# Kernel optimization log

Hardware: AMD Instinct MI355X
Metric: run time of the kernel (lower is better)

Reference implementation:

```python
import jax, jax.numpy as jnp
import numpy as np

FEATURE_DIM = 128

def setup_inputs() -> dict:
    key0 = jax.random.key(0)
    k1, k2, k3 = jax.random.split(key0, 3)
    B, NQ, NK, D = 4, 4096, 4096, FEATURE_DIM
    return {
        "target": jax.random.normal(k1, (B, NQ, D), dtype=jnp.float32),
        "key": jax.random.normal(k2, (B, NK, D), dtype=jnp.float32),
        "value": jax.random.normal(k3, (B, NK, D), dtype=jnp.float32),
    }

def reference(target, key, value):
    # Lan_K F: scores = target @ key^T / sqrt(d); weights = softmax(scores); out = weights @ value
    scale = 1.0 / np.sqrt(FEATURE_DIM).astype(np.float32)
    scores = jnp.einsum('bqd,bkd->bqk', target, key) * scale  # [B, NQ, NK]
    weights = jax.nn.softmax(scores, axis=-1)
    return jnp.einsum('bqk,bkd->bqd', weights, value)  # [B, NQ, D]
```

## Files before the change

kernel.cpp:

```cpp
#include <hip/hip_runtime.h>
#include <stdint.h>

#define B_ 4
#define NQ_ 4096
#define NK_ 4096
#define D_ 128
#define BM_ 64
#define BN_ 128
#define NITER_ (NK_/BN_)
#define KVBUF_ 32768
#define OS_ 66

typedef __attribute__((ext_vector_type(8))) short short8;
typedef __attribute__((ext_vector_type(4))) float floatx4;
typedef unsigned int u32;

union frag_u { u32 u[4]; short8 s; };

__device__ __forceinline__ unsigned short f2bf_rne(float x){
  union { float f; u32 u; } c; c.f = x;
  u32 u = c.u;
  return (unsigned short)((u + 0x7fffu + ((u >> 16) & 1u)) >> 16);
}
__device__ __forceinline__ u32 pk2bf(float a, float b){
  union { float f; u32 u; } x, y; x.f = a; y.f = b;
  u32 lo = (x.u + 0x7fffu + ((x.u >> 16) & 1u)) >> 16;
  u32 hi = (y.u + 0x7fffu + ((y.u >> 16) & 1u)) >> 16;
  return lo | (hi << 16);
}
__device__ __forceinline__ u32 pk2bf_t(float a, float b){
  union { float f; u32 u; } x, y; x.f = a; y.f = b;
  return (x.u >> 16) | (y.u & 0xffff0000u);
}

#define GLD16(gp, lp) __builtin_amdgcn_global_load_lds( \
    (const __attribute__((address_space(1))) u32*)(gp),  \
    (__attribute__((address_space(3))) u32*)(lp), 16, 0, 0)

__global__ void prep_kernel(const float* __restrict__ k, const float* __restrict__ v,
                            unsigned short* __restrict__ kb, unsigned short* __restrict__ vt){
  const int t = threadIdx.x;
  if (blockIdx.x >= 128){
    int base = (blockIdx.x - 128) * 2048 + t;
    #pragma unroll
    for (int i = 0; i < 8; i++){
      int j = base + i*256;
      float4 val = ((const float4*)k)[j];
      ushort4 s;
      s.x = f2bf_rne(val.x); s.y = f2bf_rne(val.y);
      s.z = f2bf_rne(val.z); s.w = f2bf_rne(val.w);
      ((ushort4*)kb)[j] = s;
    }
    return;
  }
  __shared__ __align__(16) float tile[128*128];
  const int b = blockIdx.x >> 5, kt = blockIdx.x & 31, k0 = kt*128;
  const float* vb = v + ((size_t)b*NK_ + k0)*D_;
  #pragma unroll
  for (int i = 0; i < 16; i++){
    int f = i*256 + t;
    int row = f >> 5, s4 = f & 31;
    *(float4*)(tile + row*128 + ((s4 ^ (row>>2)) << 2)) = *(const float4*)(vb + row*D_ + (s4<<2));
  }
  __syncthreads();
  unsigned short* vtb = vt + (size_t)b*D_*NK_ + k0;
  #pragma unroll
  for (int i = 0; i < 16; i++){
    int d = (t>>5) + 8*i, kq = t & 31;
    int s4 = d >> 2, e = d & 3;
    float v0 = tile[(4*kq+0)*128 + ((s4 ^ kq) << 2) + e];
    float v1 = tile[(4*kq+1)*128 + ((s4 ^ kq) << 2) + e];
    float v2 = tile[(4*kq+2)*128 + ((s4 ^ kq) << 2) + e];
    float v3 = tile[(4*kq+3)*128 + ((s4 ^ kq) << 2) + e];
    ushort4 o;
    o.x = f2bf_rne(v0); o.y = f2bf_rne(v1); o.z = f2bf_rne(v2); o.w = f2bf_rne(v3);
    *(ushort4*)(vtb + (size_t)d*NK_ + 4*kq) = o;
  }
}

__global__ __launch_bounds__(512, 2) void attn_kernel(
    const float* __restrict__ Qf, const unsigned short* __restrict__ Kb,
    const unsigned short* __restrict__ Vt, float* __restrict__ Out){
  __shared__ __align__(16) char sm[149504];
  char* smKb = sm;
  char* smVb = sm + 2*KVBUF_;
  char* smP  = sm + 4*KVBUF_;
  float* smL = (float*)(sm + 4*KVBUF_ + 16384);
  float* smO = (float*)sm;

  const int bi = blockIdx.x;
  const int b  = (bi >> 1) & 3;
  const int qt = ((bi >> 3) << 1) | (bi & 1);
  const int q0 = qt * BM_;
  const int tid = threadIdx.x;
  const int w = tid >> 6, lane = tid & 63;
  const int kg = w >> 1, dh = w & 1;
  const int l15 = lane & 15, l4 = lane >> 4;

  const unsigned short* kgb = Kb + (size_t)b * NK_ * D_;
  const unsigned short* vgb = Vt + (size_t)b * D_ * NK_;

  const int sr = lane >> 4;
  const int ssl = lane & 15;

  #pragma unroll
  for (int i = 0; i < 4; i++){
    int c = w*4 + i;
    int sg = ssl ^ (sr + 4*(c & 1));
    GLD16(kgb + (size_t)(c*4 + sr)*D_ + sg*8, smKb + c*1024);
    GLD16(vgb + (size_t)(c*4 + sr)*NK_ + sg*8, smVb + c*1024);
  }

  short8 qf[4][4];
  {
    const float* qp = Qf + ((size_t)b*NQ_ + q0)*D_;
    #pragma unroll
    for (int nb = 0; nb < 4; nb++)
      #pragma unroll
      for (int kb = 0; kb < 4; kb++){
        const float* p = qp + (size_t)(nb*16 + l15)*D_ + kb*32 + l4*8;
        float4 a = *(const float4*)p;
        float4 c4 = *(const float4*)(p + 4);
        frag_u f;
        f.u[0] = pk2bf(a.x, a.y);  f.u[1] = pk2bf(a.z, a.w);
        f.u[2] = pk2bf(c4.x, c4.y); f.u[3] = pk2bf(c4.z, c4.w);
        qf[nb][kb] = f.s;
      }
  }

  int koffs[4], voffs[4];
  {
    int row = kg*32 + dh*16 + l15;
    int c = row >> 2, r = row & 3, X = r + 4*(c & 1);
    #pragma unroll
    for (int k = 0; k < 4; k++)
      koffs[k] = c*1024 + r*256 + ((4*k + l4) ^ X)*16;
  }
  #pragma unroll
  for (int dt = 0; dt < 4; dt++){
    int d = dh*64 + dt*16 + l15;
    int c = d >> 2, r = d & 3, X = r + 4*(c & 1);
    voffs[dt] = c*1024 + r*256 + ((kg*4 + l4) ^ X)*16;
  }
  const int pwoff = l15*256 + (((kg*8 + dh*4 + l4) ^ (2*(l15 & 7))) * 8);
  const int proff = l15*256 + (((kg*4 + l4) ^ (l15 & 7)) * 16);

  floatx4 o[4][4];
  #pragma unroll
  for (int nb = 0; nb < 4; nb++)
    #pragma unroll
    for (int dt = 0; dt < 4; dt++) o[nb][dt] = (floatx4)0.0f;
  float lsum[4] = {0.f, 0.f, 0.f, 0.f};

  const float SL = 0.08838834764831845f * 1.4426950408889634f;

  __syncthreads();

  for (int it = 0; it < NITER_; ++it){
    const int buf = it & 1;
    char* kcur = smKb + buf * KVBUF_;
    char* vcur = smVb + buf * KVBUF_;

    if (it + 1 < NITER_){
      char* knxt = smKb + (buf ^ 1) * KVBUF_;
      #pragma unroll
      for (int i = 0; i < 4; i++){
        int c = w*4 + i;
        int sg = ssl ^ (sr + 4*(c & 1));
        GLD16(kgb + (size_t)((it+1)*BN_ + c*4 + sr)*D_ + sg*8, knxt + c*1024);
      }
    }

    short8 kf[4];
    kf[0] = *(const short8*)(kcur + koffs[0]);
    kf[1] = *(const short8*)(kcur + koffs[1]);
    kf[2] = *(const short8*)(kcur + koffs[2]);
    kf[3] = *(const short8*)(kcur + koffs[3]);
    floatx4 s[4];
    #pragma unroll
    for (int nb = 0; nb < 4; nb++){
      s[nb] = (floatx4)0.0f;
      s[nb] = __builtin_amdgcn_mfma_f32_16x16x32_bf16(kf[0], qf[nb][0], s[nb], 0,0,0);
      s[nb] = __builtin_amdgcn_mfma_f32_16x16x32_bf16(kf[1], qf[nb][1], s[nb], 0,0,0);
      s[nb] = __builtin_amdgcn_mfma_f32_16x16x32_bf16(kf[2], qf[nb][2], s[nb], 0,0,0);
      s[nb] = __builtin_amdgcn_mfma_f32_16x16x32_bf16(kf[3], qf[nb][3], s[nb], 0,0,0);
    }

    #pragma unroll
    for (int nb = 0; nb < 4; nb++){
      float p0 = __builtin_amdgcn_exp2f(s[nb][0] * SL);
      float p1 = __builtin_amdgcn_exp2f(s[nb][1] * SL);
      float p2 = __builtin_amdgcn_exp2f(s[nb][2] * SL);
      float p3 = __builtin_amdgcn_exp2f(s[nb][3] * SL);
      lsum[nb] += (p0 + p1) + (p2 + p3);
      uint2 pp; pp.x = pk2bf_t(p0, p1); pp.y = pk2bf_t(p2, p3);
      *(uint2*)(smP + nb*4096 + pwoff) = pp;
    }

    __syncthreads();

    if (it + 1 < NITER_){
      char* vnxt = smVb + (buf ^ 1) * KVBUF_;
      #pragma unroll
      for (int i = 0; i < 4; i++){
        int c = w*4 + i;
        int sg = ssl ^ (sr + 4*(c & 1));
        GLD16(vgb + (size_t)(c*4 + sr)*NK_ + (it+1)*BN_ + sg*8, vnxt + c*1024);
      }
    }

    short8 pf[4], vf[4];
    #pragma unroll
    for (int nb = 0; nb < 4; nb++)
      pf[nb] = *(const short8*)(smP + nb*4096 + proff);
    #pragma unroll
    for (int dt = 0; dt < 4; dt++)
      vf[dt] = *(const short8*)(vcur + voffs[dt]);
    #pragma unroll
    for (int nb = 0; nb < 4; nb++)
      #pragma unroll
      for (int dt = 0; dt < 4; dt++)
        o[nb][dt] = __builtin_amdgcn_mfma_f32_16x16x32_bf16(pf[nb], vf[dt], o[nb][dt], 0,0,0);

    __syncthreads();
  }

  #pragma unroll
  for (int nb = 0; nb < 4; nb++){
    float v = lsum[nb];
    v += __shfl_xor(v, 16);
    v += __shfl_xor(v, 32);
    lsum[nb] = v;
  }
  if (l4 == 0)
    #pragma unroll
    for (int nb = 0; nb < 4; nb++)
      smL[w*64 + nb*16 + l15] = lsum[nb];

  if (w >= 4){
    float* r = smO + (size_t)(w - 4) * 4224;
    #pragma unroll
    for (int nb = 0; nb < 4; nb++)
      #pragma unroll
      for (int dt = 0; dt < 4; dt++)
        #pragma unroll
        for (int q = 0; q < 4; q++)
          r[(size_t)(nb*16 + l4*4 + q)*OS_ + dt*16 + l15] = o[nb][dt][q];
  }
  __syncthreads();
  if (w < 4){
    float* r = smO + (size_t)w * 4224;
    #pragma unroll
    for (int nb = 0; nb < 4; nb++)
      #pragma unroll
      for (int dt = 0; dt < 4; dt++)
        #pragma unroll
        for (int q = 0; q < 4; q++)
          o[nb][dt][q] += r[(size_t)(nb*16 + l4*4 + q)*OS_ + dt*16 + l15];
  }
  __syncthreads();
  if (w == 2 || w == 3){
    float* r = smO + (size_t)(w - 2) * 4224;
    #pragma unroll
    for (int nb = 0; nb < 4; nb++)
      #pragma unroll
      for (int dt = 0; dt < 4; dt++)
        #pragma unroll
        for (int q = 0; q < 4; q++)
          r[(size_t)(nb*16 + l4*4 + q)*OS_ + dt*16 + l15] = o[nb][dt][q];
  }
  __syncthreads();
  if (w < 2){
    float* r = smO + (size_t)w * 4224;
    float* og = Out + ((size_t)b*NQ_ + q0)*D_ + dh*64;
    #pragma unroll
    for (int nb = 0; nb < 4; nb++)
      #pragma unroll
      for (int q = 0; q < 4; q++){
        int row = nb*16 + l4*4 + q;
        float lt = 0.f;
        #pragma unroll
        for (int w2 = 0; w2 < 8; w2++) lt += smL[w2*64 + row];
        float inv = 1.0f / lt;
        #pragma unroll
        for (int dt = 0; dt < 4; dt++){
          float val = o[nb][dt][q] + r[(size_t)row*OS_ + dt*16 + l15];
          og[(size_t)row*D_ + dt*16 + l15] = val * inv;
        }
      }
  }
}

extern "C" void kernel_launch(void* const* d_in, const int* in_sizes, int n_in,
                              void* d_out, int out_size, void* d_ws, size_t ws_size,
                              hipStream_t stream){
  const float* q = (const float*)d_in[0];
  const float* k = (const float*)d_in[1];
  const float* v = (const float*)d_in[2];
  float* out = (float*)d_out;
  unsigned short* kb = (unsigned short*)d_ws;
  unsigned short* vt = kb + (size_t)B_*NK_*D_;
  prep_kernel<<<384, 256, 0, stream>>>(k, v, kb, vt);
  attn_kernel<<<256, 512, 0, stream>>>(q, kb, vt, out);
}
```

Measured before the change: 133.6 us.

## Drop LDS staging; load K/V MFMA fragments directly from global memory

```diff
diff --git a/kernel.cpp b/kernel.cpp
--- a/kernel.cpp
+++ b/kernel.cpp
@@ -5,11 +5,7 @@
 #define NQ_ 4096
 #define NK_ 4096
 #define D_ 128
-#define BM_ 64
-#define BN_ 128
-#define NITER_ (NK_/BN_)
-#define KVBUF_ 32768
-#define OS_ 66
+#define NITER_ 16
 
 typedef __attribute__((ext_vector_type(8))) short short8;
 typedef __attribute__((ext_vector_type(4))) float floatx4;
@@ -33,10 +29,7 @@
   return (x.u >> 16) | (y.u & 0xffff0000u);
 }
 
-#define GLD16(gp, lp) __builtin_amdgcn_global_load_lds( \
-    (const __attribute__((address_space(1))) u32*)(gp),  \
-    (__attribute__((address_space(3))) u32*)(lp), 16, 0, 0)
-
+#define TS_ 136
 __global__ void prep_kernel(const float* __restrict__ k, const float* __restrict__ v,
                             unsigned short* __restrict__ kb, unsigned short* __restrict__ vt){
   const int t = threadIdx.x;
@@ -66,7 +59,8 @@
   unsigned short* vtb = vt + (size_t)b*D_*NK_ + k0;
   #pragma unroll
   for (int i = 0; i < 16; i++){
-    int d = (t>>5) + 8*i, kq = t & 31;
+    int u2 = t >> 5, kq = t & 31;
+    int d = u2 + 8*i;
     int s4 = d >> 2, e = d & 3;
     float v0 = tile[(4*kq+0)*128 + ((s4 ^ kq) << 2) + e];
     float v1 = tile[(4*kq+1)*128 + ((s4 ^ kq) << 2) + e];
@@ -81,35 +75,16 @@
 __global__ __launch_bounds__(512, 2) void attn_kernel(
     const float* __restrict__ Qf, const unsigned short* __restrict__ Kb,
     const unsigned short* __restrict__ Vt, float* __restrict__ Out){
-  __shared__ __align__(16) char sm[149504];
-  char* smKb = sm;
-  char* smVb = sm + 2*KVBUF_;
-  char* smP  = sm + 4*KVBUF_;
-  float* smL = (float*)(sm + 4*KVBUF_ + 16384);
-  float* smO = (float*)sm;
+  __shared__ __align__(16) float smO[4][64*132];
+  __shared__ float smL[8*64 + 64];
 
   const int bi = blockIdx.x;
   const int b  = (bi >> 1) & 3;
   const int qt = ((bi >> 3) << 1) | (bi & 1);
-  const int q0 = qt * BM_;
+  const int q0 = qt * 64;
   const int tid = threadIdx.x;
   const int w = tid >> 6, lane = tid & 63;
-  const int kg = w >> 1, dh = w & 1;
   const int l15 = lane & 15, l4 = lane >> 4;
-
-  const unsigned short* kgb = Kb + (size_t)b * NK_ * D_;
-  const unsigned short* vgb = Vt + (size_t)b * D_ * NK_;
-
-  const int sr = lane >> 4;
-  const int ssl = lane & 15;
-
-  #pragma unroll
-  for (int i = 0; i < 4; i++){
-    int c = w*4 + i;
-    int sg = ssl ^ (sr + 4*(c & 1));
-    GLD16(kgb + (size_t)(c*4 + sr)*D_ + sg*8, smKb + c*1024);
-    GLD16(vgb + (size_t)(c*4 + sr)*NK_ + sg*8, smVb + c*1024);
-  }
 
   short8 qf[4][4];
   {
@@ -128,101 +103,68 @@
       }
   }
 
-  int koffs[4], voffs[4];
-  {
-    int row = kg*32 + dh*16 + l15;
-    int c = row >> 2, r = row & 3, X = r + 4*(c & 1);
-    #pragma unroll
-    for (int k = 0; k < 4; k++)
-      koffs[k] = c*1024 + r*256 + ((4*k + l4) ^ X)*16;
-  }
-  #pragma unroll
-  for (int dt = 0; dt < 4; dt++){
-    int d = dh*64 + dt*16 + l15;
-    int c = d >> 2, r = d & 3, X = r + 4*(c & 1);
-    voffs[dt] = c*1024 + r*256 + ((kg*4 + l4) ^ X)*16;
-  }
-  const int pwoff = l15*256 + (((kg*8 + dh*4 + l4) ^ (2*(l15 & 7))) * 8);
-  const int proff = l15*256 + (((kg*4 + l4) ^ (l15 & 7)) * 16);
-
-  floatx4 o[4][4];
+  const char* kit = (const char*)Kb + (size_t)b*((size_t)NK_*D_*2)
+                  + (size_t)((w*32 + (l15&3) + ((l15>>2)<<3))*256 + l4*16);
+  const char* vit = (const char*)Vt + (size_t)b*((size_t)D_*NK_*2)
+                  + (size_t)(l15*(NK_*2) + w*64 + l4*16);
+
+  floatx4 o[4][8];
   #pragma unroll
   for (int nb = 0; nb < 4; nb++)
     #pragma unroll
-    for (int dt = 0; dt < 4; dt++) o[nb][dt] = (floatx4)0.0f;
+    for (int nd = 0; nd < 8; nd++) o[nb][nd] = (floatx4)0.0f;
   float lsum[4] = {0.f, 0.f, 0.f, 0.f};
 
   const float SL = 0.08838834764831845f * 1.4426950408889634f;
 
-  __syncthreads();
-
   for (int it = 0; it < NITER_; ++it){
-    const int buf = it & 1;
-    char* kcur = smKb + buf * KVBUF_;
-    char* vcur = smVb + buf * KVBUF_;
-
-    if (it + 1 < NITER_){
-      char* knxt = smKb + (buf ^ 1) * KVBUF_;
-      #pragma unroll
-      for (int i = 0; i < 4; i++){
-        int c = w*4 + i;
-        int sg = ssl ^ (sr + 4*(c & 1));
-        GLD16(kgb + (size_t)((it+1)*BN_ + c*4 + sr)*D_ + sg*8, knxt + c*1024);
+    short8 vf[8];
+    vf[0] = *(const short8*)(vit + 0*(size_t)(16*NK_*2));
+    vf[1] = *(const short8*)(vit + 1*(size_t)(16*NK_*2));
+    vf[2] = *(const short8*)(vit + 2*(size_t)(16*NK_*2));
+    vf[3] = *(const short8*)(vit + 3*(size_t)(16*NK_*2));
+
+    frag_u pa[4];
+    #pragma unroll
+    for (int g = 0; g < 2; g++){
+      short8 kf[4];
+      kf[0] = *(const short8*)(kit + g*1024 + 0);
+      kf[1] = *(const short8*)(kit + g*1024 + 64);
+      kf[2] = *(const short8*)(kit + g*1024 + 128);
+      kf[3] = *(const short8*)(kit + g*1024 + 192);
+      floatx4 s[4];
+      #pragma unroll
+      for (int nb = 0; nb < 4; nb++){
+        s[nb] = (floatx4)0.0f;
+        s[nb] = __builtin_amdgcn_mfma_f32_16x16x32_bf16(kf[0], qf[nb][0], s[nb], 0,0,0);
+        s[nb] = __builtin_amdgcn_mfma_f32_16x16x32_bf16(kf[1], qf[nb][1], s[nb], 0,0,0);
+        s[nb] = __builtin_amdgcn_mfma_f32_16x16x32_bf16(kf[2], qf[nb][2], s[nb], 0,0,0);
+        s[nb] = __builtin_amdgcn_mfma_f32_16x16x32_bf16(kf[3], qf[nb][3], s[nb], 0,0,0);
+      }
+      #pragma unroll
+      for (int nb = 0; nb < 4; nb++){
+        float p0 = __builtin_amdgcn_exp2f(s[nb][0] * SL);
+        float p1 = __builtin_amdgcn_exp2f(s[nb][1] * SL);
+        float p2 = __builtin_amdgcn_exp2f(s[nb][2] * SL);
+        float p3 = __builtin_amdgcn_exp2f(s[nb][3] * SL);
+        lsum[nb] += (p0 + p1) + (p2 + p3);
+        pa[nb].u[2*g + 0] = pk2bf_t(p0, p1);
+        pa[nb].u[2*g + 1] = pk2bf_t(p2, p3);
       }
     }
-
-    short8 kf[4];
-    kf[0] = *(const short8*)(kcur + koffs[0]);
-    kf[1] = *(const short8*)(kcur + koffs[1]);
-    kf[2] = *(const short8*)(kcur + koffs[2]);
-    kf[3] = *(const short8*)(kcur + koffs[3]);
-    floatx4 s[4];
-    #pragma unroll
-    for (int nb = 0; nb < 4; nb++){
-      s[nb] = (floatx4)0.0f;
-      s[nb] = __builtin_amdgcn_mfma_f32_16x16x32_bf16(kf[0], qf[nb][0], s[nb], 0,0,0);
-      s[nb] = __builtin_amdgcn_mfma_f32_16x16x32_bf16(kf[1], qf[nb][1], s[nb], 0,0,0);
-      s[nb] = __builtin_amdgcn_mfma_f32_16x16x32_bf16(kf[2], qf[nb][2], s[nb], 0,0,0);
-      s[nb] = __builtin_amdgcn_mfma_f32_16x16x32_bf16(kf[3], qf[nb][3], s[nb], 0,0,0);
-    }
-
-    #pragma unroll
-    for (int nb = 0; nb < 4; nb++){
-      float p0 = __builtin_amdgcn_exp2f(s[nb][0] * SL);
-      float p1 = __builtin_amdgcn_exp2f(s[nb][1] * SL);
-      float p2 = __builtin_amdgcn_exp2f(s[nb][2] * SL);
-      float p3 = __builtin_amdgcn_exp2f(s[nb][3] * SL);
-      lsum[nb] += (p0 + p1) + (p2 + p3);
-      uint2 pp; pp.x = pk2bf_t(p0, p1); pp.y = pk2bf_t(p2, p3);
-      *(uint2*)(smP + nb*4096 + pwoff) = pp;
-    }
-
-    __syncthreads();
-
-    if (it + 1 < NITER_){
-      char* vnxt = smVb + (buf ^ 1) * KVBUF_;
-      #pragma unroll
-      for (int i = 0; i < 4; i++){
-        int c = w*4 + i;
-        int sg = ssl ^ (sr + 4*(c & 1));
-        GLD16(vgb + (size_t)(c*4 + sr)*NK_ + (it+1)*BN_ + sg*8, vnxt + c*1024);
-      }
-    }
-
-    short8 pf[4], vf[4];
-    #pragma unroll
-    for (int nb = 0; nb < 4; nb++)
-      pf[nb] = *(const short8*)(smP + nb*4096 + proff);
-    #pragma unroll
-    for (int dt = 0; dt < 4; dt++)
-      vf[dt] = *(const short8*)(vcur + voffs[dt]);
-    #pragma unroll
-    for (int nb = 0; nb < 4; nb++)
-      #pragma unroll
-      for (int dt = 0; dt < 4; dt++)
-        o[nb][dt] = __builtin_amdgcn_mfma_f32_16x16x32_bf16(pf[nb], vf[dt], o[nb][dt], 0,0,0);
-
-    __syncthreads();
+    vf[4] = *(const short8*)(vit + 4*(size_t)(16*NK_*2));
+    vf[5] = *(const short8*)(vit + 5*(size_t)(16*NK_*2));
+    vf[6] = *(const short8*)(vit + 6*(size_t)(16*NK_*2));
+    vf[7] = *(const short8*)(vit + 7*(size_t)(16*NK_*2));
+
+    #pragma unroll
+    for (int nb = 0; nb < 4; nb++)
+      #pragma unroll
+      for (int nd = 0; nd < 8; nd++)
+        o[nb][nd] = __builtin_amdgcn_mfma_f32_16x16x32_bf16(pa[nb].s, vf[nd], o[nb][nd], 0,0,0);
+
+    kit += 65536;
+    vit += 512;
   }
 
   #pragma unroll
@@ -230,62 +172,94 @@
     float v = lsum[nb];
     v += __shfl_xor(v, 16);
     v += __shfl_xor(v, 32);
-    lsum[nb] = v;
-  }
-  if (l4 == 0)
-    #pragma unroll
-    for (int nb = 0; nb < 4; nb++)
-      smL[w*64 + nb*16 + l15] = lsum[nb];
-
+    if (l4 == 0) smL[w*64 + nb*16 + l15] = v;
+  }
   if (w >= 4){
-    float* r = smO + (size_t)(w - 4) * 4224;
-    #pragma unroll
-    for (int nb = 0; nb < 4; nb++)
-      #pragma unroll
-      for (int dt = 0; dt < 4; dt++)
-        #pragma unroll
-        for (int q = 0; q < 4; q++)
-          r[(size_t)(nb*16 + l4*4 + q)*OS_ + dt*16 + l15] = o[nb][dt][q];
+    float* r = smO[w - 4];
+    #pragma unroll
+    for (int nb = 0; nb < 4; nb++)
+      #pragma unroll
+      for (int nd = 0; nd < 8; nd++)
+        #pragma unroll
+        for (int q = 0; q < 4; q++)
+          r[(nb*16 + l4*4 + q)*132 + nd*16 + l15] = o[nb][nd][q];
   }
   __syncthreads();
   if (w < 4){
-    float* r = smO + (size_t)w * 4224;
-    #pragma unroll
-    for (int nb = 0; nb < 4; nb++)
-      #pragma unroll
-      for (int dt = 0; dt < 4; dt++)
-        #pragma unroll
-        for (int q = 0; q < 4; q++)
-          o[nb][dt][q] += r[(size_t)(nb*16 + l4*4 + q)*OS_ + dt*16 + l15];
+    const float* r = smO[w];
+    #pragma unroll
+    for (int nb = 0; nb < 4; nb++)
+      #pragma unroll
+      for (int nd = 0; nd < 8; nd++)
+        #pragma unroll
+        for (int q = 0; q < 4; q++)
+          o[nb][nd][q] += r[(nb*16 + l4*4 + q)*132 + nd*16 + l15];
+  }
+  if (tid < 64){
+    float t = 0.f;
+    #pragma unroll
+    for (int w2 = 0; w2 < 8; w2++) t += smL[w2*64 + tid];
+    smL[512 + tid] = t;
   }
   __syncthreads();
   if (w == 2 || w == 3){
-    float* r = smO + (size_t)(w - 2) * 4224;
-    #pragma unroll
-    for (int nb = 0; nb < 4; nb++)
-      #pragma unroll
-      for (int dt = 0; dt < 4; dt++)
-        #pragma unroll
-        for (int q = 0; q < 4; q++)
-          r[(size_t)(nb*16 + l4*4 + q)*OS_ + dt*16 + l15] = o[nb][dt][q];
+    float* r = smO[w - 2];
+    #pragma unroll
+    for (int nb = 0; nb < 4; nb++)
+      #pragma unroll
+      for (int nd = 0; nd < 8; nd++)
+        #pragma unroll
+        for (int q = 0; q < 4; q++)
+          r[(nb*16 + l4*4 + q)*132 + nd*16 + l15] = o[nb][nd][q];
   }
   __syncthreads();
   if (w < 2){
-    float* r = smO + (size_t)w * 4224;
-    float* og = Out + ((size_t)b*NQ_ + q0)*D_ + dh*64;
+    const float* r = smO[w];
+    #pragma unroll
+    for (int nb = 0; nb < 4; nb++)
+      #pragma unroll
+      for (int nd = 0; nd < 8; nd++)
+        #pragma unroll
+        for (int q = 0; q < 4; q++)
+          o[nb][nd][q] += r[(nb*16 + l4*4 + q)*132 + nd*16 + l15];
+  }
+  __syncthreads();
+  if (w == 1){
+    float* r = smO[0];
+    #pragma unroll
+    for (int nb = 0; nb < 4; nb++)
+      #pragma unroll
+      for (int nd = 0; nd < 4; nd++)
+        #pragma unroll
+        for (int q = 0; q < 4; q++)
+          r[(nb*16 + l4*4 + q)*132 + nd*16 + l15] = o[nb][nd][q];
+  }
+  if (w == 0){
+    float* r = smO[1];
+    #pragma unroll
+    for (int nb = 0; nb < 4; nb++)
+      #pragma unroll
+      for (int nd = 4; nd < 8; nd++)
+        #pragma unroll
+        for (int q = 0; q < 4; q++)
+          r[(nb*16 + l4*4 + q)*132 + nd*16 + l15] = o[nb][nd][q];
+  }
+  __syncthreads();
+  if (w < 2){
+    const float* r = smO[w];
+    float* og = Out + ((size_t)b*NQ_ + q0)*D_;
+    const int nd0 = w * 4;
     #pragma unroll
     for (int nb = 0; nb < 4; nb++)
       #pragma unroll
       for (int q = 0; q < 4; q++){
         int row = nb*16 + l4*4 + q;
-        float lt = 0.f;
-        #pragma unroll
-        for (int w2 = 0; w2 < 8; w2++) lt += smL[w2*64 + row];
-        float inv = 1.0f / lt;
-        #pragma unroll
-        for (int dt = 0; dt < 4; dt++){
-          float val = o[nb][dt][q] + r[(size_t)row*OS_ + dt*16 + l15];
-          og[(size_t)row*D_ + dt*16 + l15] = val * inv;
+        float inv = 1.0f / smL[512 + row];
+        #pragma unroll
+        for (int nd2 = 0; nd2 < 4; nd2++){
+          int nd = nd0 + nd2;
+          float val = o[nb][nd][q] + r[row*132 + nd*16 + l15];
+          og[(size_t)row*D_ + nd*16 + l15] = val * inv;
         }
       }
   }
```

Result: slower. 196.6 us (+47.1%).
